# Performance work log

Hardware: AMD Instinct MI355X
Metric: run time of the kernel (lower is better)

The kernel has to match this reference:

```python
import jax, jax.numpy as jnp
import numpy as np

WEIGHT_THRESH = 0.5
EPS = 1e-5


def setup_inputs() -> dict:
    key = jax.random.key(0)
    k1, k2, k3 = jax.random.split(key, 3)
    B, N = 4096, 2048
    src_points = jax.random.normal(k1, (B, N, 3), dtype=jnp.float32)
    tgt_points = jax.random.normal(k2, (B, N, 3), dtype=jnp.float32)
    weights = jax.random.uniform(k3, (B, N), dtype=jnp.float32)
    return {"src_points": src_points, "tgt_points": tgt_points, "weights": weights}


def reference(src_points, tgt_points, weights):
    # threshold + normalize weights: (B, N)
    w = jnp.where(weights < WEIGHT_THRESH, jnp.zeros_like(weights), weights)
    w = w / (jnp.sum(w, axis=1, keepdims=True) + EPS)
    w = w[:, :, None]  # (B, N, 1)

    # weighted centroids (B, 1, 3)
    src_centroid = jnp.sum(src_points * w, axis=1, keepdims=True)
    ref_centroid = jnp.sum(tgt_points * w, axis=1, keepdims=True)
    src_c = src_points - src_centroid
    ref_c = tgt_points - ref_centroid

    # cross-covariance H = src_c^T @ (w * ref_c): (B, 3, 3)
    H = jnp.einsum("bnd,bne->bde", src_c, w * ref_c)

    U, _, Vh = jnp.linalg.svd(H)
    V = jnp.swapaxes(Vh, -1, -2)
    Ut = jnp.swapaxes(U, -1, -2)

    # sign correction: R = V @ diag(1,1,sign(det(V Ut))) @ Ut
    s = jnp.sign(jnp.linalg.det(V @ Ut))  # (B,)
    d = jnp.stack([jnp.ones_like(s), jnp.ones_like(s), s], axis=-1)  # (B, 3)
    R = (V * d[:, None, :]) @ Ut  # scale columns of V

    t = ref_centroid[:, 0, :] - jnp.einsum("bij,bj->bi", R, src_centroid[:, 0, :])
    return R, t
```

## Files before the change

### kernel.cpp

```cpp
#include <hip/hip_runtime.h>
#include <math.h>

#define NPTS 2048
#define THREADS 256


__device__ inline void acc4(const float4 wq, const float4 s0, const float4 s1,
                            const float4 s2, const float4 t0, const float4 t1,
                            const float4 t2, float acc[16])
{
    const float wv[4]  = {wq.x, wq.y, wq.z, wq.w};
    const float sv[12] = {s0.x, s0.y, s0.z, s0.w, s1.x, s1.y,
                          s1.z, s1.w, s2.x, s2.y, s2.z, s2.w};
    const float tv[12] = {t0.x, t0.y, t0.z, t0.w, t1.x, t1.y,
                          t1.z, t1.w, t2.x, t2.y, t2.z, t2.w};
#pragma unroll
    for (int k = 0; k < 4; ++k) {
        const float wvk = (wv[k] < 0.5f) ? 0.f : wv[k];
        const float sx = sv[3 * k + 0], sy = sv[3 * k + 1], sz = sv[3 * k + 2];
        const float tx = tv[3 * k + 0], ty = tv[3 * k + 1], tz = tv[3 * k + 2];
        const float wsx = wvk * sx, wsy = wvk * sy, wsz = wvk * sz;
        acc[0] += wvk;
        acc[1] += wsx; acc[2] += wsy; acc[3] += wsz;
        acc[4] += wvk * tx; acc[5] += wvk * ty; acc[6] += wvk * tz;
        acc[7]  += wsx * tx; acc[8]  += wsx * ty; acc[9]  += wsx * tz;
        acc[10] += wsy * tx; acc[11] += wsy * ty; acc[12] += wsy * tz;
        acc[13] += wsz * tx; acc[14] += wsz * ty; acc[15] += wsz * tz;
    }
}

template <int M, int HALF>
__device__ inline void bflevel(float acc[16], int lane)
{
    const bool hi = lane & M;
#pragma unroll
    for (int j = 0; j < HALF; ++j) {
        const float keep = hi ? acc[j + HALF] : acc[j];
        const float send = hi ? acc[j] : acc[j + HALF];
        acc[j] = keep + __shfl_xor(send, M, 64);
    }
}

__global__ __launch_bounds__(THREADS, 4) void wp_reduce_kernel(
    const float* __restrict__ src, const float* __restrict__ tgt,
    const float* __restrict__ w, float* __restrict__ ws)
{
    const int b = blockIdx.x;
    const int tid = threadIdx.x;
    const float* sp = src + (size_t)b * NPTS * 3;
    const float* tp = tgt + (size_t)b * NPTS * 3;
    const float* wp = w + (size_t)b * NPTS;

    const int nA = tid * 4;
    const int nB = 1024 + tid * 4;

    const float4 wqA = *reinterpret_cast<const float4*>(wp + nA);
    const float4 wqB = *reinterpret_cast<const float4*>(wp + nB);
    const float4* sA = reinterpret_cast<const float4*>(sp + 3 * nA);
    const float4 sA0 = sA[0], sA1 = sA[1], sA2 = sA[2];
    const float4* sB = reinterpret_cast<const float4*>(sp + 3 * nB);
    const float4 sB0 = sB[0], sB1 = sB[1], sB2 = sB[2];
    const float4* tA = reinterpret_cast<const float4*>(tp + 3 * nA);
    const float4 tA0 = tA[0], tA1 = tA[1], tA2 = tA[2];
    const float4* tB = reinterpret_cast<const float4*>(tp + 3 * nB);
    const float4 tB0 = tB[0], tB1 = tB[1], tB2 = tB[2];
    __builtin_amdgcn_sched_barrier(0);

    float acc[16];
#pragma unroll
    for (int i = 0; i < 16; ++i) acc[i] = 0.f;

    acc4(wqA, sA0, sA1, sA2, tA0, tA1, tA2, acc);
    acc4(wqB, sB0, sB1, sB2, tB0, tB1, tB2, acc);

    const int wave = tid >> 6;
    const int lane = tid & 63;
    bflevel<1, 8>(acc, lane);
    bflevel<2, 4>(acc, lane);
    bflevel<4, 2>(acc, lane);
    bflevel<8, 1>(acc, lane);
    acc[0] += __shfl_xor(acc[0], 16, 64);
    acc[0] += __shfl_xor(acc[0], 32, 64);

    __shared__ float lds[4][16];
    if (lane < 16) {
        const int idx = ((lane & 1) << 3) | ((lane & 2) << 1) |
                        ((lane & 4) >> 1) | ((lane & 8) >> 3);
        lds[wave][idx] = acc[0];
    }
    __syncthreads();
    if (tid < 16) {
        const float v = lds[0][tid] + lds[1][tid] + lds[2][tid] + lds[3][tid];
        ws[(size_t)b * 16 + tid] = v;
    }
}


template <int P, int Q>
__device__ inline void jrot(double A[3][3], double V[3][3])
{
    const double apq = A[P][Q];
    if (fabs(apq) < 1e-300) return;
    const double theta = (A[Q][Q] - A[P][P]) / (2.0 * apq);
    const double t = ((theta >= 0.0) ? 1.0 : -1.0) /
                     (fabs(theta) + sqrt(theta * theta + 1.0));
    const double c = 1.0 / sqrt(t * t + 1.0);
    const double s = t * c;
#pragma unroll
    for (int k = 0; k < 3; ++k) {
        const double akp = A[k][P], akq = A[k][Q];
        A[k][P] = c * akp - s * akq;
        A[k][Q] = s * akp + c * akq;
    }
#pragma unroll
    for (int k = 0; k < 3; ++k) {
        const double apk = A[P][k], aqk = A[Q][k];
        A[P][k] = c * apk - s * aqk;
        A[Q][k] = s * apk + c * aqk;
    }
#pragma unroll
    for (int k = 0; k < 3; ++k) {
        const double vkp = V[k][P], vkq = V[k][Q];
        V[k][P] = c * vkp - s * vkq;
        V[k][Q] = s * vkp + c * vkq;
    }
}

__device__ inline void matvec3(const double H[3][3], const double v[3], double u[3])
{
#pragma unroll
    for (int i = 0; i < 3; ++i)
        u[i] = H[i][0] * v[0] + H[i][1] * v[1] + H[i][2] * v[2];
}

__device__ inline double dot3(const double a[3], const double b[3])
{
    return a[0] * b[0] + a[1] * b[1] + a[2] * b[2];
}

__device__ inline void cross3(const double a[3], const double b[3], double c[3])
{
    c[0] = a[1] * b[2] - a[2] * b[1];
    c[1] = a[2] * b[0] - a[0] * b[2];
    c[2] = a[0] * b[1] - a[1] * b[0];
}

__global__ void wp_svd_kernel(const float* __restrict__ ws, float* __restrict__ out,
                              int B)
{
    const int b = blockIdx.x * blockDim.x + threadIdx.x;
    if (b >= B) return;

    float s16[16];
#pragma unroll
    for (int i = 0; i < 16; ++i) s16[i] = ws[(size_t)b * 16 + i];

    const double Sw = (double)s16[0];
    const double D = Sw + 1e-5;
    const double invD = 1.0 / D;
    double sc[3], tc[3];
#pragma unroll
    for (int i = 0; i < 3; ++i) {
        sc[i] = (double)s16[1 + i] * invD;
        tc[i] = (double)s16[4 + i] * invD;
    }
    const double f = 2.0 - Sw * invD;

    double H[3][3];
#pragma unroll
    for (int d = 0; d < 3; ++d)
#pragma unroll
        for (int e = 0; e < 3; ++e)
            H[d][e] = (double)s16[7 + 3 * d + e] * invD - sc[d] * tc[e] * f;

    double A[3][3];
#pragma unroll
    for (int i = 0; i < 3; ++i)
#pragma unroll
        for (int j = 0; j < 3; ++j)
            A[i][j] = H[0][i] * H[0][j] + H[1][i] * H[1][j] + H[2][i] * H[2][j];

    double V[3][3] = {{1, 0, 0}, {0, 1, 0}, {0, 0, 1}};
#pragma unroll
    for (int sweep = 0; sweep < 5; ++sweep) {
        jrot<0, 1>(A, V);
        jrot<0, 2>(A, V);
        jrot<1, 2>(A, V);
    }

    const double l0 = A[0][0], l1 = A[1][1], l2 = A[2][2];
    int i0 = 0; double lm = l0;
    if (l1 > lm) { lm = l1; i0 = 1; }
    if (l2 > lm) { lm = l2; i0 = 2; }
    int i2 = 0; double ls = l0;
    if (l1 < ls) { ls = l1; i2 = 1; }
    if (l2 < ls) { ls = l2; i2 = 2; }
    if (i2 == i0) i2 = (i0 + 1) % 3;
    const int i1 = 3 - i0 - i2;

    double v1[3], v2[3], v3[3];
#pragma unroll
    for (int k = 0; k < 3; ++k) {
        v1[k] = V[k][i0];
        v2[k] = V[k][i1];
        v3[k] = V[k][i2];
    }

    double u1[3], u2[3], u3[3];
    matvec3(H, v1, u1);
    const double n1 = sqrt(dot3(u1, u1));
    const double inv1 = 1.0 / fmax(n1, 1e-300);
#pragma unroll
    for (int k = 0; k < 3; ++k) u1[k] *= inv1;

    matvec3(H, v2, u2);
    const double d12 = dot3(u2, u1);
#pragma unroll
    for (int k = 0; k < 3; ++k) u2[k] -= d12 * u1[k];
    double n2 = sqrt(dot3(u2, u2));
    if (n2 < 1e-14 * fmax(n1, 1e-300)) {
        double ax[3] = {1.0, 0.0, 0.0};
        if (fabs(u1[0]) > 0.9) { ax[0] = 0.0; ax[1] = 1.0; }
        cross3(u1, ax, u2);
        n2 = sqrt(dot3(u2, u2));
    }
    const double inv2 = 1.0 / fmax(n2, 1e-300);
#pragma unroll
    for (int k = 0; k < 3; ++k) u2[k] *= inv2;
    cross3(u1, u2, u3);

    double cr[3];
    cross3(v2, v3, cr);
    const double detV = dot3(v1, cr);
    const double s3 = (detV < 0.0) ? -1.0 : 1.0;

    double R[3][3];
#pragma unroll
    for (int i = 0; i < 3; ++i)
#pragma unroll
        for (int j = 0; j < 3; ++j)
            R[i][j] = v1[i] * u1[j] + v2[i] * u2[j] + s3 * v3[i] * u3[j];

    double t[3];
#pragma unroll
    for (int i = 0; i < 3; ++i)
        t[i] = tc[i] - (R[i][0] * sc[0] + R[i][1] * sc[1] + R[i][2] * sc[2]);

    float* outR = out + (size_t)b * 9;
#pragma unroll
    for (int i = 0; i < 3; ++i)
#pragma unroll
        for (int j = 0; j < 3; ++j)
            outR[3 * i + j] = (float)R[i][j];
    float* outT = out + (size_t)B * 9 + (size_t)b * 3;
#pragma unroll
    for (int i = 0; i < 3; ++i) outT[i] = (float)t[i];
}

extern "C" void kernel_launch(void* const* d_in, const int* in_sizes, int n_in,
                              void* d_out, int out_size, void* d_ws, size_t ws_size,
                              hipStream_t stream)
{
    const float* src = (const float*)d_in[0];
    const float* tgt = (const float*)d_in[1];
    const float* w   = (const float*)d_in[2];
    float* out = (float*)d_out;
    float* ws  = (float*)d_ws;
    const int B = in_sizes[2] / NPTS;

    wp_reduce_kernel<<<B, THREADS, 0, stream>>>(src, tgt, w, ws);
    wp_svd_kernel<<<(B + 63) / 64, 64, 0, stream>>>(ws, out, B);
}
```

Baseline: 45.50 us.

## Stage point data through LDS with fully coalesced float4 loads

The reduction kernel now loads src and tgt with lane-contiguous float4 reads (stride 256 float4s) into 48 KB of shared memory, then each thread reads its points' xyz from LDS with stride-3 scalar accesses. Weights are read as scalar coalesced loads. This replaces the per-thread 48-byte strided float4 global loads, aiming for better global coalescing. The cost is an extra LDS round trip, a barrier, and fewer resident blocks because of the large shared allocation. Launch bounds also drop from 4 to 3 blocks per SM.

```diff
diff --git a/kernel.cpp b/kernel.cpp
--- a/kernel.cpp
+++ b/kernel.cpp
@@ -5,20 +5,67 @@
 #define THREADS 256
 
 
-__device__ inline void acc4(const float4 wq, const float4 s0, const float4 s1,
-                            const float4 s2, const float4 t0, const float4 t1,
-                            const float4 t2, float acc[16])
-{
-    const float wv[4]  = {wq.x, wq.y, wq.z, wq.w};
-    const float sv[12] = {s0.x, s0.y, s0.z, s0.w, s1.x, s1.y,
-                          s1.z, s1.w, s2.x, s2.y, s2.z, s2.w};
-    const float tv[12] = {t0.x, t0.y, t0.z, t0.w, t1.x, t1.y,
-                          t1.z, t1.w, t2.x, t2.y, t2.z, t2.w};
-#pragma unroll
-    for (int k = 0; k < 4; ++k) {
-        const float wvk = (wv[k] < 0.5f) ? 0.f : wv[k];
-        const float sx = sv[3 * k + 0], sy = sv[3 * k + 1], sz = sv[3 * k + 2];
-        const float tx = tv[3 * k + 0], ty = tv[3 * k + 1], tz = tv[3 * k + 2];
+template <int M, int HALF>
+__device__ inline void bflevel(float acc[16], int lane)
+{
+    const bool hi = lane & M;
+#pragma unroll
+    for (int j = 0; j < HALF; ++j) {
+        const float keep = hi ? acc[j + HALF] : acc[j];
+        const float send = hi ? acc[j] : acc[j + HALF];
+        acc[j] = keep + __shfl_xor(send, M, 64);
+    }
+}
+
+__global__ __launch_bounds__(THREADS, 3) void wp_reduce_kernel(
+    const float* __restrict__ src, const float* __restrict__ tgt,
+    const float* __restrict__ w, float* __restrict__ ws)
+{
+    const int b = blockIdx.x;
+    const int tid = threadIdx.x;
+    const float* sp = src + (size_t)b * NPTS * 3;
+    const float* tp = tgt + (size_t)b * NPTS * 3;
+    const float* wp = w + (size_t)b * NPTS;
+
+    __shared__ float lsrc[NPTS * 3];
+    __shared__ float ltgt[NPTS * 3];
+    __shared__ float lpart[4][16];
+
+    const float4* s4 = reinterpret_cast<const float4*>(sp);
+    const float4* t4 = reinterpret_cast<const float4*>(tp);
+    float4* ls4 = reinterpret_cast<float4*>(lsrc);
+    float4* lt4 = reinterpret_cast<float4*>(ltgt);
+
+    float4 rs[6], rt[6];
+#pragma unroll
+    for (int j = 0; j < 6; ++j) rs[j] = s4[tid + 256 * j];
+#pragma unroll
+    for (int j = 0; j < 6; ++j) rt[j] = t4[tid + 256 * j];
+
+    float wv8[8];
+#pragma unroll
+    for (int k = 0; k < 8; ++k) wv8[k] = wp[tid + 256 * k];
+
+#pragma unroll
+    for (int j = 0; j < 6; ++j) ls4[tid + 256 * j] = rs[j];
+#pragma unroll
+    for (int j = 0; j < 6; ++j) lt4[tid + 256 * j] = rt[j];
+    __syncthreads();
+
+    float acc[16];
+#pragma unroll
+    for (int i = 0; i < 16; ++i) acc[i] = 0.f;
+
+#pragma unroll
+    for (int k = 0; k < 8; ++k) {
+        const int n = tid + 256 * k;
+        const float wvk = (wv8[k] < 0.5f) ? 0.f : wv8[k];
+        const float sx = lsrc[3 * n + 0];
+        const float sy = lsrc[3 * n + 1];
+        const float sz = lsrc[3 * n + 2];
+        const float tx = ltgt[3 * n + 0];
+        const float ty = ltgt[3 * n + 1];
+        const float tz = ltgt[3 * n + 2];
         const float wsx = wvk * sx, wsy = wvk * sy, wsz = wvk * sz;
         acc[0] += wvk;
         acc[1] += wsx; acc[2] += wsy; acc[3] += wsz;
@@ -27,51 +74,6 @@
         acc[10] += wsy * tx; acc[11] += wsy * ty; acc[12] += wsy * tz;
         acc[13] += wsz * tx; acc[14] += wsz * ty; acc[15] += wsz * tz;
     }
-}
-
-template <int M, int HALF>
-__device__ inline void bflevel(float acc[16], int lane)
-{
-    const bool hi = lane & M;
-#pragma unroll
-    for (int j = 0; j < HALF; ++j) {
-        const float keep = hi ? acc[j + HALF] : acc[j];
-        const float send = hi ? acc[j] : acc[j + HALF];
-        acc[j] = keep + __shfl_xor(send, M, 64);
-    }
-}
-
-__global__ __launch_bounds__(THREADS, 4) void wp_reduce_kernel(
-    const float* __restrict__ src, const float* __restrict__ tgt,
-    const float* __restrict__ w, float* __restrict__ ws)
-{
-    const int b = blockIdx.x;
-    const int tid = threadIdx.x;
-    const float* sp = src + (size_t)b * NPTS * 3;
-    const float* tp = tgt + (size_t)b * NPTS * 3;
-    const float* wp = w + (size_t)b * NPTS;
-
-    const int nA = tid * 4;
-    const int nB = 1024 + tid * 4;
-
-    const float4 wqA = *reinterpret_cast<const float4*>(wp + nA);
-    const float4 wqB = *reinterpret_cast<const float4*>(wp + nB);
-    const float4* sA = reinterpret_cast<const float4*>(sp + 3 * nA);
-    const float4 sA0 = sA[0], sA1 = sA[1], sA2 = sA[2];
-    const float4* sB = reinterpret_cast<const float4*>(sp + 3 * nB);
-    const float4 sB0 = sB[0], sB1 = sB[1], sB2 = sB[2];
-    const float4* tA = reinterpret_cast<const float4*>(tp + 3 * nA);
-    const float4 tA0 = tA[0], tA1 = tA[1], tA2 = tA[2];
-    const float4* tB = reinterpret_cast<const float4*>(tp + 3 * nB);
-    const float4 tB0 = tB[0], tB1 = tB[1], tB2 = tB[2];
-    __builtin_amdgcn_sched_barrier(0);
-
-    float acc[16];
-#pragma unroll
-    for (int i = 0; i < 16; ++i) acc[i] = 0.f;
-
-    acc4(wqA, sA0, sA1, sA2, tA0, tA1, tA2, acc);
-    acc4(wqB, sB0, sB1, sB2, tB0, tB1, tB2, acc);
 
     const int wave = tid >> 6;
     const int lane = tid & 63;
@@ -82,15 +84,14 @@
     acc[0] += __shfl_xor(acc[0], 16, 64);
     acc[0] += __shfl_xor(acc[0], 32, 64);
 
-    __shared__ float lds[4][16];
     if (lane < 16) {
         const int idx = ((lane & 1) << 3) | ((lane & 2) << 1) |
                         ((lane & 4) >> 1) | ((lane & 8) >> 3);
-        lds[wave][idx] = acc[0];
+        lpart[wave][idx] = acc[0];
     }
     __syncthreads();
     if (tid < 16) {
-        const float v = lds[0][tid] + lds[1][tid] + lds[2][tid] + lds[3][tid];
+        const float v = lpart[0][tid] + lpart[1][tid] + lpart[2][tid] + lpart[3][tid];
         ws[(size_t)b * 16 + tid] = v;
     }
 }
```

Result: slower. 46.62 us (+2.5%).
